# Performance work log

Hardware: AMD Instinct MI355X
Metric: run time of the kernel (lower is better)

## Reference

```python
import jax, jax.numpy as jnp
import numpy as np

B, N, DIM, H = 2, 4096, 1024, 16
LAT = 1024
CTX = N - LAT            # 3072 context tokens
SEG = 12                 # num_segments
CHUNK = CTX // SEG       # 256 tokens per segment
D = DIM // H             # 64 head dim
SCALE = D ** -0.5
LN_EPS = 1e-5
NEG = float(-np.finfo(np.float32).max)


def _split_heads(t):  # [B, N, DIM] -> [(B*H), N, D]
    return t.reshape(B, N, H, D).transpose(0, 2, 1, 3).reshape(B * H, N, D)


def _merge_heads(t):  # [(B*H), n, D] -> [B, n, DIM]
    n = t.shape[1]
    return t.reshape(B, H, n, D).transpose(0, 2, 1, 3).reshape(B, n, DIM)


def _layernorm(t, g, b):  # LN over last dim (head dim)
    mu = t.mean(-1, keepdims=True)
    var = ((t - mu) ** 2).mean(-1, keepdims=True)
    return (t - mu) * jax.lax.rsqrt(var + LN_EPS) * g + b


def _rope(t):  # rotary embedding over full head dim, half-split rotate
    pos = jnp.arange(N, dtype=jnp.float32)
    inv = 1.0 / (10000.0 ** (jnp.arange(0, D, 2, dtype=jnp.float32) / D))
    freqs = pos[:, None] * inv[None, :]          # [N, D/2]
    emb = jnp.concatenate([freqs, freqs], -1)    # [N, D]
    cos, sin = jnp.cos(emb), jnp.sin(emb)
    rot = jnp.concatenate([-t[..., D // 2:], t[..., : D // 2]], -1)
    return t * cos + rot * sin


def setup_inputs() -> dict:
    key = jax.random.key(0)
    ks = jax.random.split(key, 4)
    s = 0.02
    return {
        "x": jax.random.normal(ks[0], (B, N, DIM), jnp.float32),
        "Wq": jax.random.normal(ks[1], (DIM, DIM), jnp.float32) * s,
        "Wkv": jax.random.normal(ks[2], (DIM, DIM), jnp.float32) * s,
        "Wo": jax.random.normal(ks[3], (DIM, DIM), jnp.float32) * s,
        "bo": jnp.zeros((DIM,), jnp.float32),
        "ln_g": jnp.ones((D,), jnp.float32),
        "ln_b": jnp.zeros((D,), jnp.float32),
    }


def reference(x, Wq, Wkv, Wo, bo, ln_g, ln_b):
    q = _split_heads(x @ Wq)    # [(BH), N, D]
    kv = _split_heads(x @ Wkv)  # [(BH), N, D]
    q, kv = _rope(q), _rope(kv)

    lkv = _layernorm(kv, ln_g, ln_b)  # normalized keys/values, full seq

    q_lat = q[:, CTX:] * SCALE                                   # [(BH), LAT, D]
    q_ctx = (q[:, :CTX] * SCALE).reshape(B * H, SEG, CHUNK, D)   # segmented ctx queries
    lkv_ctx = lkv[:, :CTX].reshape(B * H, SEG, CHUNK, D)         # segmented norm'd kv

    # latent queries: full attention over all N positions, causal among latents
    lsim = jnp.einsum('bid,bjd->bij', q_lat, lkv)                # [(BH), LAT, N]
    tri = jnp.triu(jnp.ones((LAT, LAT), bool), 1)
    lat_block = jnp.where(tri, NEG, lsim[:, :, CTX:])
    lsim = jnp.concatenate([lsim[:, :, :CTX], lat_block], axis=-1)
    attn = jax.nn.softmax(lsim, axis=-1)
    out_lat = jnp.einsum('bij,bjd->bid', attn, lkv)              # [(BH), LAT, D]

    # context queries: block-diagonal segmented local attention (non-causal)
    sim_ctx = jnp.einsum('bsid,bsjd->bsij', q_ctx, lkv_ctx)      # [(BH), SEG, CHUNK, CHUNK]
    attn_ctx = jax.nn.softmax(sim_ctx, axis=-1)
    out_ctx = jnp.einsum('bsij,bsjd->bsid', attn_ctx, lkv_ctx).reshape(B * H, CTX, D)

    out = jnp.concatenate([_merge_heads(out_ctx), _merge_heads(out_lat)], axis=1)
    return out @ Wo + bo
```

## Files before the change

### kernel.cpp

```cpp
#include <hip/hip_runtime.h>
#include <math.h>

#define NB_B 2
#define NB_N 4096
#define NB_DIM 1024
#define NB_H 16
#define NB_D 64
#define NB_CTX 3072
#define NSPLIT 4
#define QSCALE 0.18033688011112042f
#define NEGF -3.0e38f

typedef __attribute__((ext_vector_type(8))) short short8;
typedef __attribute__((ext_vector_type(4))) short s4v;
typedef __attribute__((ext_vector_type(4))) float f32x4;

#if __has_builtin(__builtin_amdgcn_mfma_f32_16x16x16bf16_1k)
__device__ __forceinline__ f32x4 mfma16(s4v a, s4v b, f32x4 c) {
  return __builtin_amdgcn_mfma_f32_16x16x16bf16_1k(a, b, c, 0, 0, 0);
}
#else
__device__ __forceinline__ f32x4 mfma16(s4v a, s4v b, f32x4 c) {
  f32x4 d;
  asm volatile("v_mfma_f32_16x16x16_bf16 %0, %1, %2, %3"
               : "=v"(d) : "v"(a), "v"(b), "v"(c));
  return d;
}
#endif

__device__ __forceinline__ unsigned short f2bf(float f) {
  union { float f; unsigned u; } v; v.f = f;
  unsigned r = v.u + 0x7fffu + ((v.u >> 16) & 1u);
  return (unsigned short)(r >> 16);
}

__device__ __forceinline__ unsigned int cvtpk(float a, float b) {
  unsigned int r;
  asm("v_cvt_pk_bf16_f32 %0, %1, %2" : "=v"(r) : "v"(a), "v"(b));
  return r;
}

__device__ __forceinline__ void async16(const void* g, void* l) {
  typedef const unsigned int __attribute__((address_space(1)))* gas_t;
  typedef unsigned int __attribute__((address_space(3)))* las_t;
  __builtin_amdgcn_global_load_lds((gas_t)(unsigned long long)g,
                                   (las_t)(unsigned)(unsigned long long)l,
                                   16, 0, 0);
}

__global__ __launch_bounds__(256) void k_prep(
    const float* __restrict__ x,
    const float* __restrict__ Wq, const float* __restrict__ Wkv, const float* __restrict__ Wo,
    unsigned short* __restrict__ xb, unsigned short* __restrict__ WqkvT,
    unsigned short* __restrict__ WoT, float2* __restrict__ tab)
{
  __shared__ float tile[64][65];
  const int bx = blockIdx.x, tid = threadIdx.x;
  if (bx < 2048) {
    const float4* x4 = (const float4*)x;
    ushort4* xb4 = (ushort4*)xb;
    const int n4 = (NB_B * NB_N * NB_DIM) / 4;
    for (int i = bx * 256 + tid; i < n4; i += 2048 * 256) {
      float4 v = x4[i];
      ushort4 o;
      o.x = f2bf(v.x); o.y = f2bf(v.y); o.z = f2bf(v.z); o.w = f2bf(v.w);
      xb4[i] = o;
    }
  } else if (bx < 2816) {
    int idx = bx - 2048;
    int z = idx >> 8, rem = idx & 255;
    const float* W; unsigned short* out;
    if (z == 0)      { W = Wq;  out = WqkvT; }
    else if (z == 1) { W = Wkv; out = WqkvT + 1024 * 1024; }
    else             { W = Wo;  out = WoT; }
    int c0 = (rem & 15) * 64, k0 = (rem >> 4) * 64;
    int tx = tid & 63, ty = tid >> 6;
    #pragma unroll
    for (int i = 0; i < 16; ++i) {
      int k = ty + i * 4;
      tile[k][tx] = W[(long)(k0 + k) * 1024 + c0 + tx];
    }
    __syncthreads();
    #pragma unroll
    for (int i = 0; i < 16; ++i) {
      int c = ty + i * 4;
      out[(long)(c0 + c) * 1024 + k0 + tx] = f2bf(tile[tx][c]);
    }
  } else {
    int idx = (bx - 2816) * 256 + tid;
    int n = idx >> 5, fi = idx & 31;
    float inv = exp2f(-(float)fi * (13.287712379549449f / 32.0f));
    float ang = (float)n * inv;
    float s, c;
    sincosf(ang, &s, &c);
    tab[idx] = make_float2(c, s);
  }
}

__global__ __launch_bounds__(256) void k_gemm_qkv(
    const unsigned short* __restrict__ A,
    const unsigned short* __restrict__ Bt,
    unsigned short* __restrict__ qf,
    unsigned short* __restrict__ lkvp,
    const float2* __restrict__ tab,
    const float* __restrict__ ln_g,
    const float* __restrict__ ln_b)
{
  __shared__ unsigned short As[128 * 32];
  __shared__ unsigned short Bs[128 * 32];
  const int tid = threadIdx.x;
  const int w = tid >> 6, lane = tid & 63;
  const int wr = w >> 1, wc = w & 1;
  const int quad = lane >> 4, l15 = lane & 15;
  const long tm = (long)blockIdx.y * 128, tn = (long)blockIdx.x * 128;
  const int K = 1024;

  f32x4 acc[4][4];
  #pragma unroll
  for (int i = 0; i < 4; ++i)
    #pragma unroll
    for (int j = 0; j < 4; ++j)
      acc[i][j] = (f32x4){0.f, 0.f, 0.f, 0.f};

  const unsigned short* Ag0 = A + (tm + w * 16 + (lane >> 2)) * K + (lane & 3) * 8;
  const unsigned short* Bg0 = Bt + (tn + w * 16 + (lane >> 2)) * K + (lane & 3) * 8;
  const unsigned short* Ag1 = Ag0 + (long)64 * K;
  const unsigned short* Bg1 = Bg0 + (long)64 * K;
  unsigned short* Al0 = &As[(w * 16) * 32];
  unsigned short* Al1 = &As[(64 + w * 16) * 32];
  unsigned short* Bl0 = &Bs[(w * 16) * 32];
  unsigned short* Bl1 = &Bs[(64 + w * 16) * 32];

  for (int k0 = 0; k0 < K; k0 += 32) {
    __syncthreads();
    async16(Ag0 + k0, Al0);
    async16(Ag1 + k0, Al1);
    async16(Bg0 + k0, Bl0);
    async16(Bg1 + k0, Bl1);
    __syncthreads();
    short8 af[4], bfr[4];
    #pragma unroll
    for (int i = 0; i < 4; ++i)
      af[i] = *(const short8*)&As[(wr * 64 + i * 16 + l15) * 32 + quad * 8];
    #pragma unroll
    for (int j = 0; j < 4; ++j)
      bfr[j] = *(const short8*)&Bs[(wc * 64 + j * 16 + l15) * 32 + quad * 8];
    #pragma unroll
    for (int i = 0; i < 4; ++i)
      #pragma unroll
      for (int j = 0; j < 4; ++j)
        acc[i][j] = __builtin_amdgcn_mfma_f32_16x16x32_bf16(af[i], bfr[j], acc[i][j], 0, 0, 0);
  }

  const int col_base = (int)tn + wc * 64;
  const bool is_q = col_base < 1024;
  const int hh = (col_base & 1023) >> 6;
  unsigned short* dst = is_q ? qf : lkvp;
  float g_ln[4], b_ln[4];
  #pragma unroll
  for (int j = 0; j < 4; ++j) { g_ln[j] = ln_g[j * 16 + l15]; b_ln[j] = ln_b[j * 16 + l15]; }

  const int row_base = (int)tm + wr * 64;
  #pragma unroll
  for (int i = 0; i < 4; ++i) {
    #pragma unroll
    for (int r = 0; r < 4; ++r) {
      const int row = row_base + i * 16 + quad * 4 + r;
      const int n = row & 4095, b = row >> 12;
      const float2 cs0 = tab[n * 32 + l15];
      const float2 cs1 = tab[n * 32 + 16 + l15];
      float val[4];
      #pragma unroll
      for (int j = 0; j < 4; ++j) {
        float t = acc[i][j][r], pt = acc[i][j ^ 2][r];
        float2 cs = (j & 1) ? cs1 : cs0;
        float rot = (j < 2) ? -pt : pt;
        val[j] = t * cs.x + rot * cs.y;
      }
      unsigned short* orow = dst + ((long)(b * 16 + hh) * NB_N + n) * 64;
      if (is_q) {
        #pragma unroll
        for (int j = 0; j < 4; ++j)
          orow[j * 16 + l15] = f2bf(val[j] * QSCALE);
      } else {
        float s = val[0] + val[1] + val[2] + val[3];
        #pragma unroll
        for (int o = 1; o < 16; o <<= 1) s += __shfl_xor(s, o);
        const float mu = s * 0.015625f;
        float dv[4], vs = 0.f;
        #pragma unroll
        for (int j = 0; j < 4; ++j) { dv[j] = val[j] - mu; vs += dv[j] * dv[j]; }
        #pragma unroll
        for (int o = 1; o < 16; o <<= 1) vs += __shfl_xor(vs, o);
        const float rr = rsqrtf(vs * 0.015625f + 1e-5f);
        #pragma unroll
        for (int j = 0; j < 4; ++j)
          orow[j * 16 + l15] = f2bf(dv[j] * rr * g_ln[j] + b_ln[j]);
      }
    }
  }
}

__global__ __launch_bounds__(256) void k_gemm_bt(
    const unsigned short* __restrict__ A,
    const unsigned short* __restrict__ Bt,
    float* __restrict__ C,
    const float* __restrict__ bias,
    int K, int ldc)
{
  __shared__ unsigned short As[128 * 32];
  __shared__ unsigned short Bs[128 * 32];
  const int tid = threadIdx.x;
  const int w = tid >> 6, lane = tid & 63;
  const int wr = w >> 1, wc = w & 1;
  const int quad = lane >> 4, l15 = lane & 15;
  const long tm = (long)blockIdx.y * 128, tn = (long)blockIdx.x * 128;

  f32x4 acc[4][4];
  #pragma unroll
  for (int i = 0; i < 4; ++i)
    #pragma unroll
    for (int j = 0; j < 4; ++j)
      acc[i][j] = (f32x4){0.f, 0.f, 0.f, 0.f};

  const unsigned short* Ag0 = A + (tm + w * 16 + (lane >> 2)) * K + (lane & 3) * 8;
  const unsigned short* Bg0 = Bt + (tn + w * 16 + (lane >> 2)) * K + (lane & 3) * 8;
  const unsigned short* Ag1 = Ag0 + (long)64 * K;
  const unsigned short* Bg1 = Bg0 + (long)64 * K;
  unsigned short* Al0 = &As[(w * 16) * 32];
  unsigned short* Al1 = &As[(64 + w * 16) * 32];
  unsigned short* Bl0 = &Bs[(w * 16) * 32];
  unsigned short* Bl1 = &Bs[(64 + w * 16) * 32];

  for (int k0 = 0; k0 < K; k0 += 32) {
    __syncthreads();
    async16(Ag0 + k0, Al0);
    async16(Ag1 + k0, Al1);
    async16(Bg0 + k0, Bl0);
    async16(Bg1 + k0, Bl1);
    __syncthreads();
    short8 af[4], bfr[4];
    #pragma unroll
    for (int i = 0; i < 4; ++i)
      af[i] = *(const short8*)&As[(wr * 64 + i * 16 + l15) * 32 + quad * 8];
    #pragma unroll
    for (int j = 0; j < 4; ++j)
      bfr[j] = *(const short8*)&Bs[(wc * 64 + j * 16 + l15) * 32 + quad * 8];
    #pragma unroll
    for (int i = 0; i < 4; ++i)
      #pragma unroll
      for (int j = 0; j < 4; ++j)
        acc[i][j] = __builtin_amdgcn_mfma_f32_16x16x32_bf16(af[i], bfr[j], acc[i][j], 0, 0, 0);
  }

  #pragma unroll
  for (int j = 0; j < 4; ++j) {
    const long col = tn + wc * 64 + j * 16 + l15;
    const float bv = bias ? bias[col] : 0.0f;
    #pragma unroll
    for (int i = 0; i < 4; ++i) {
      #pragma unroll
      for (int r = 0; r < 4; ++r) {
        const long row = tm + wr * 64 + i * 16 + quad * 4 + r;
        C[row * ldc + col] = acc[i][j][r] + bv;
      }
    }
  }
}


__device__ __forceinline__ void stage_kv(
    unsigned short* __restrict__ Ksn, unsigned short* __restrict__ Vtn,
    const int kp, const int sdc, const uint4& gA, const uint4& gB)
{
  *(uint4*)&Ksn[(2 * kp) * 72 + sdc * 8] = gA;
  *(uint4*)&Ksn[(2 * kp + 1) * 72 + sdc * 8] = gB;
  const unsigned int* wA = (const unsigned int*)&gA;
  const unsigned int* wB = (const unsigned int*)&gB;
  #pragma unroll
  for (int jw = 0; jw < 4; ++jw) {
    const unsigned int lo = __builtin_amdgcn_perm(wB[jw], wA[jw], 0x05040100u);
    const unsigned int hi = __builtin_amdgcn_perm(wB[jw], wA[jw], 0x07060302u);
    const int d0 = sdc * 8 + jw * 2;
    const int xo = (2 * kp) ^ (d0 & 56);
    *(unsigned int*)&Vtn[d0 * 72 + xo] = lo;
    *(unsigned int*)&Vtn[(d0 + 1) * 72 + xo] = hi;
  }
}

#define NB_PACK(QG, SUB)                                               \
  _Pragma("unroll")                                                    \
  for (int k4 = 0; k4 < 4; ++k4) {                                     \
    const float p0 = __builtin_amdgcn_exp2f(st[QG][k4][0] SUB);        \
    const float p1 = __builtin_amdgcn_exp2f(st[QG][k4][1] SUB);        \
    const float p2 = __builtin_amdgcn_exp2f(st[QG][k4][2] SUB);        \
    const float p3 = __builtin_amdgcn_exp2f(st[QG][k4][3] SUB);        \
    pk[QG][k4][0] = cvtpk(p0, p1);                                     \
    pk[QG][k4][1] = cvtpk(p2, p3);                                     \
  }

__device__ __forceinline__ void attn_tile(
    const unsigned short* __restrict__ Ks, const unsigned short* __restrict__ Vt,
    unsigned short* __restrict__ Ksn, unsigned short* __restrict__ Vtn,
    const int kt, const int kt1, const int kstart, const bool latent, const int q0lat,
    const int w, const int quad, const int l15, const int kp, const int sdc,
    const unsigned short* __restrict__ kbase,
    uint4& gA, uint4& gB, const short8 (&qfr)[2][2],
    f32x4 (&ot)[2][4], f32x4 (&lacc)[2], float& miu, float& thr)
{
  const int key0 = kstart + kt * 64;
  __syncthreads();

  if (kt + 1 < kt1) {
    stage_kv(Ksn, Vtn, kp, sdc, gA, gB);
    if (kt + 2 < kt1) {
      const long k2 = (long)(key0 + 128);
      gA = *(const uint4*)(kbase + (k2 + 2 * kp) * 64 + sdc * 8);
      gB = *(const uint4*)(kbase + (k2 + 2 * kp + 1) * 64 + sdc * 8);
    }
  }

  f32x4 st[2][4];
  #pragma unroll
  for (int qg = 0; qg < 2; ++qg)
    #pragma unroll
    for (int k4 = 0; k4 < 4; ++k4)
      st[qg][k4] = (f32x4){0.f, 0.f, 0.f, 0.f};
  #pragma unroll
  for (int kc = 0; kc < 2; ++kc) {
    short8 kf[4];
    #pragma unroll
    for (int k4 = 0; k4 < 4; ++k4)
      kf[k4] = *(const short8*)&Ks[(k4 * 16 + l15) * 72 + kc * 32 + quad * 8];
    #pragma unroll
    for (int qg = 0; qg < 2; ++qg)
      #pragma unroll
      for (int k4 = 0; k4 < 4; ++k4)
        st[qg][k4] = __builtin_amdgcn_mfma_f32_16x16x32_bf16(kf[k4], qfr[qg][kc], st[qg][k4], 0, 0, 0);
  }

  if (latent && key0 + 63 >= NB_CTX) {
    #pragma unroll
    for (int qg = 0; qg < 2; ++qg) {
      const int qrow = q0lat + w * 32 + qg * 16 + l15;
      #pragma unroll
      for (int k4 = 0; k4 < 4; ++k4)
        #pragma unroll
        for (int r = 0; r < 4; ++r) {
          const int kl = key0 + k4 * 16 + quad * 4 + r - NB_CTX;
          if (kl > qrow) st[qg][k4][r] = NEGF;
        }
    }
  }

  float mx = st[0][0][0];
  #pragma unroll
  for (int qg = 0; qg < 2; ++qg)
    #pragma unroll
    for (int k4 = 0; k4 < 4; ++k4)
      mx = fmaxf(mx, fmaxf(fmaxf(st[qg][k4][0], st[qg][k4][1]),
                           fmaxf(st[qg][k4][2], st[qg][k4][3])));

  unsigned int pk[2][4][2];
  if (miu == 0.f) {
    NB_PACK(0, )
    NB_PACK(1, )
  } else {
    NB_PACK(0, - miu)
    NB_PACK(1, - miu)
  }

  const s4v vones = { (short)0x3F80, (short)0x3F80, (short)0x3F80, (short)0x3F80 };
  #pragma unroll
  for (int k4 = 0; k4 < 4; ++k4) {
    s4v vf[4];
    const int kb = k4 * 16 + quad * 4;
    #pragma unroll
    for (int dt = 0; dt < 4; ++dt) {
      const int row = dt * 16 + l15;
      vf[dt] = *(const s4v*)&Vt[row * 72 + (kb ^ (row & 56))];
    }
    #pragma unroll
    for (int qg = 0; qg < 2; ++qg) {
      s4v pf;
      ((unsigned int*)&pf)[0] = pk[qg][k4][0];
      ((unsigned int*)&pf)[1] = pk[qg][k4][1];
      lacc[qg] = mfma16(vones, pf, lacc[qg]);
      #pragma unroll
      for (int dt = 0; dt < 4; ++dt)
        ot[qg][dt] = mfma16(vf[dt], pf, ot[qg][dt]);
    }
  }

  if (__builtin_expect(__any(mx > thr), 0)) {
    #pragma unroll
    for (int o = 1; o < 64; o <<= 1) mx = fmaxf(mx, __shfl_xor(mx, o));
    const float c = __builtin_amdgcn_exp2f(miu - mx);
    miu = mx; thr = mx + 8.f;
    #pragma unroll
    for (int qg = 0; qg < 2; ++qg) {
      lacc[qg][0] *= c; lacc[qg][1] *= c; lacc[qg][2] *= c; lacc[qg][3] *= c;
      #pragma unroll
      for (int dt = 0; dt < 4; ++dt) {
        ot[qg][dt][0] *= c; ot[qg][dt][1] *= c;
        ot[qg][dt][2] *= c; ot[qg][dt][3] *= c;
      }
    }
  }
}

__global__ __launch_bounds__(256) void k_attn(
    const unsigned short* __restrict__ qf,
    const unsigned short* __restrict__ lkv,
    unsigned short* __restrict__ attn_out,
    float* __restrict__ Opart,
    float* __restrict__ mpart,
    float* __restrict__ lpart)
{
  __shared__ unsigned short smem[18432];
  unsigned short* const Ks0 = smem;
  unsigned short* const Vt0 = smem + 4608;
  unsigned short* const Ks1 = smem + 9216;
  unsigned short* const Vt1 = smem + 13824;

  const int tid = threadIdx.x;
  const int w = tid >> 6, lane = tid & 63;
  const int quad = lane >> 4, l15 = lane & 15;

  const int bx = blockIdx.x;
  int bh, q0tok, kstart, kt0, kt1, q0lat, s6 = 0, qb = 0;
  bool latent;
  if (bx < 256 * NSPLIT) {
    latent = true;
    qb = bx / NSPLIT;
    s6 = bx % NSPLIT;
    bh = qb >> 3;
    q0lat = (qb & 7) * 128;
    q0tok = NB_CTX + q0lat;
    kstart = 0;
    const int nkt = (NB_CTX + q0lat + 128) >> 6;
    const int hk = nkt >> 1;
    kt0 = 2 * ((s6 * hk) / NSPLIT);
    kt1 = 2 * (((s6 + 1) * hk) / NSPLIT);
  } else {
    latent = false;
    int idx = bx - 256 * NSPLIT;
    bh = idx / 24;
    int r2 = idx % 24;
    int seg = r2 >> 1;
    q0lat = 0;
    q0tok = seg * 256 + (r2 & 1) * 128;
    kstart = seg * 256;
    kt0 = 0; kt1 = 4;
  }

  const unsigned short* qbase = qf + ((long)bh * NB_N + q0tok) * 64;
  const unsigned short* kbase = lkv + (long)bh * NB_N * 64;

  short8 qfr[2][2];
  #pragma unroll
  for (int qg = 0; qg < 2; ++qg)
    #pragma unroll
    for (int kc = 0; kc < 2; ++kc)
      qfr[qg][kc] = *(const short8*)(qbase + (w * 32 + qg * 16 + l15) * 64 + kc * 32 + quad * 8);

  const int kp = tid >> 3, sdc = tid & 7;

  uint4 gA, gB;
  {
    const int key0 = kstart + kt0 * 64;
    gA = *(const uint4*)(kbase + (long)(key0 + 2 * kp) * 64 + sdc * 8);
    gB = *(const uint4*)(kbase + (long)(key0 + 2 * kp + 1) * 64 + sdc * 8);
  }
  stage_kv(Ks0, Vt0, kp, sdc, gA, gB);
  {
    const int key1 = kstart + (kt0 + 1) * 64;
    gA = *(const uint4*)(kbase + (long)(key1 + 2 * kp) * 64 + sdc * 8);
    gB = *(const uint4*)(kbase + (long)(key1 + 2 * kp + 1) * 64 + sdc * 8);
  }

  f32x4 ot[2][4];
  f32x4 lacc[2];
  float miu = 0.f, thr = 8.f;
  #pragma unroll
  for (int qg = 0; qg < 2; ++qg) {
    #pragma unroll
    for (int dt = 0; dt < 4; ++dt) ot[qg][dt] = (f32x4){0.f, 0.f, 0.f, 0.f};
    lacc[qg] = (f32x4){0.f, 0.f, 0.f, 0.f};
  }

  for (int kt = kt0; kt < kt1; kt += 2) {
    attn_tile(Ks0, Vt0, Ks1, Vt1, kt,     kt1, kstart, latent, q0lat,
              w, quad, l15, kp, sdc, kbase, gA, gB, qfr, ot, lacc, miu, thr);
    attn_tile(Ks1, Vt1, Ks0, Vt0, kt + 1, kt1, kstart, latent, q0lat,
              w, quad, l15, kp, sdc, kbase, gA, gB, qfr, ot, lacc, miu, thr);
  }

  __syncthreads();
  if (latent) {
    const long pb = (long)(s6 * 256 + qb);
    if (quad == 0) {
      #pragma unroll
      for (int qg = 0; qg < 2; ++qg) {
        mpart[pb * 128 + w * 32 + qg * 16 + l15] = miu;
        lpart[pb * 128 + w * 32 + qg * 16 + l15] = lacc[qg][0];
      }
    }
    float* obase = Opart + pb * 8192;
    #pragma unroll
    for (int qg = 0; qg < 2; ++qg) {
      const int q = w * 32 + qg * 16 + l15;
      #pragma unroll
      for (int dt = 0; dt < 4; ++dt)
        #pragma unroll
        for (int r = 0; r < 4; ++r)
          obase[(dt * 16 + quad * 4 + r) * 128 + q] = ot[qg][dt][r];
    }
  } else {
    #pragma unroll
    for (int qg = 0; qg < 2; ++qg) {
      const float inv = 1.0f / lacc[qg][0];
      const int q = w * 32 + qg * 16 + l15;
      #pragma unroll
      for (int dt = 0; dt < 4; ++dt)
        #pragma unroll
        for (int r = 0; r < 4; ++r)
          smem[q * 72 + dt * 16 + quad * 4 + r] = f2bf(ot[qg][dt][r] * inv);
    }
    __syncthreads();
    const int qrow = tid >> 1, half = tid & 1;
    const int b_ = bh >> 4, h_ = bh & 15;
    unsigned short* orow = attn_out + ((long)b_ * NB_N + q0tok + qrow) * NB_DIM + h_ * 64 + half * 32;
    #pragma unroll
    for (int v = 0; v < 4; ++v)
      *(uint4*)(orow + v * 8) = *(const uint4*)&smem[qrow * 72 + half * 32 + v * 8];
  }
}

__global__ __launch_bounds__(256) void k_combine(
    const float* __restrict__ Opart, const float* __restrict__ mpart,
    const float* __restrict__ lpart, unsigned short* __restrict__ attn_out)
{
  __shared__ unsigned short lds[9216];
  const int qb = blockIdx.x;
  const int bh = qb >> 3, qt = qb & 7;
  const int b = bh >> 4, h = bh & 15;
  const int t = threadIdx.x;
  const int qq = t & 31;
  const int dg = t >> 5;

  float m[NSPLIT][4], l[NSPLIT][4];
  float mstar[4];
  #pragma unroll
  for (int qi = 0; qi < 4; ++qi) mstar[qi] = NEGF;
  #pragma unroll
  for (int s = 0; s < NSPLIT; ++s) {
    #pragma unroll
    for (int qi = 0; qi < 4; ++qi) {
      m[s][qi] = mpart[(s * 256 + qb) * 128 + qq * 4 + qi];
      l[s][qi] = lpart[(s * 256 + qb) * 128 + qq * 4 + qi];
      mstar[qi] = fmaxf(mstar[qi], m[s][qi]);
    }
  }
  float inv[4];
  #pragma unroll
  for (int qi = 0; qi < 4; ++qi) {
    float lsum = 0.f;
    #pragma unroll
    for (int s = 0; s < NSPLIT; ++s)
      lsum += __builtin_amdgcn_exp2f(m[s][qi] - mstar[qi]) * l[s][qi];
    inv[qi] = 1.0f / lsum;
  }

  float o[8][4];
  #pragma unroll
  for (int dd = 0; dd < 8; ++dd)
    #pragma unroll
    for (int qi = 0; qi < 4; ++qi) o[dd][qi] = 0.f;
  #pragma unroll
  for (int s = 0; s < NSPLIT; ++s) {
    float wgt[4];
    #pragma unroll
    for (int qi = 0; qi < 4; ++qi)
      wgt[qi] = __builtin_amdgcn_exp2f(m[s][qi] - mstar[qi]);
    const float* base = Opart + (long)(s * 256 + qb) * 8192;
    #pragma unroll
    for (int dd = 0; dd < 8; ++dd) {
      float4 v = *(const float4*)(base + (dg * 8 + dd) * 128 + qq * 4);
      o[dd][0] += wgt[0] * v.x; o[dd][1] += wgt[1] * v.y;
      o[dd][2] += wgt[2] * v.z; o[dd][3] += wgt[3] * v.w;
    }
  }
  #pragma unroll
  for (int qi = 0; qi < 4; ++qi) {
    ushort4 u0, u1;
    u0.x = f2bf(o[0][qi] * inv[qi]); u0.y = f2bf(o[1][qi] * inv[qi]);
    u0.z = f2bf(o[2][qi] * inv[qi]); u0.w = f2bf(o[3][qi] * inv[qi]);
    u1.x = f2bf(o[4][qi] * inv[qi]); u1.y = f2bf(o[5][qi] * inv[qi]);
    u1.z = f2bf(o[6][qi] * inv[qi]); u1.w = f2bf(o[7][qi] * inv[qi]);
    *(ushort4*)&lds[(qq * 4 + qi) * 72 + dg * 8] = u0;
    *(ushort4*)&lds[(qq * 4 + qi) * 72 + dg * 8 + 4] = u1;
  }
  __syncthreads();
  const int qrow = t >> 1, half = t & 1;
  unsigned short* orow = attn_out + ((long)b * NB_N + NB_CTX + qt * 128 + qrow) * NB_DIM + h * 64 + half * 32;
  #pragma unroll
  for (int v = 0; v < 4; ++v)
    *(uint4*)(orow + v * 8) = *(const uint4*)&lds[qrow * 72 + half * 32 + v * 8];
}

extern "C" void kernel_launch(void* const* d_in, const int* in_sizes, int n_in,
                              void* d_out, int out_size, void* d_ws, size_t ws_size,
                              hipStream_t stream)
{
  const float* x    = (const float*)d_in[0];
  const float* Wq   = (const float*)d_in[1];
  const float* Wkv  = (const float*)d_in[2];
  const float* Wo   = (const float*)d_in[3];
  const float* bo   = (const float*)d_in[4];
  const float* ln_g = (const float*)d_in[5];
  const float* ln_b = (const float*)d_in[6];
  float* out = (float*)d_out;

  char* ws = (char*)d_ws;
  unsigned short* xb    = (unsigned short*)(ws);
  unsigned short* WqkvT = (unsigned short*)(ws + (size_t)(16 << 20));
  unsigned short* WoT   = (unsigned short*)(ws + (size_t)(20 << 20));
  float2*         tab   = (float2*)        (ws + (size_t)(22 << 20));
  unsigned short* qfb   = (unsigned short*)(ws + (size_t)(24 << 20));
  unsigned short* lkv   = (unsigned short*)(ws + (size_t)(40 << 20));
  unsigned short* aout  = (unsigned short*)(ws + (size_t)(56 << 20));
  float*          Opart = (float*)         (ws + (size_t)(72 << 20));
  float*          mpart = (float*)         (ws + (size_t)(112 << 20));
  float*          lpart = (float*)         (ws + (size_t)(113 << 20));

  hipLaunchKernelGGL(k_prep, dim3(3328), dim3(256), 0, stream,
                     x, Wq, Wkv, Wo, xb, WqkvT, WoT, tab);
  hipLaunchKernelGGL(k_gemm_qkv, dim3(16, 64), dim3(256), 0, stream,
                     xb, WqkvT, qfb, lkv, tab, ln_g, ln_b);
  hipLaunchKernelGGL(k_attn, dim3(256 * NSPLIT + 768), dim3(256), 0, stream,
                     qfb, lkv, aout, Opart, mpart, lpart);
  hipLaunchKernelGGL(k_combine, dim3(256), dim3(256), 0, stream,
                     Opart, mpart, lpart, aout);
  hipLaunchKernelGGL(k_gemm_bt, dim3(8, 64), dim3(256), 0, stream,
                     aout, WoT, out, bo, 1024, 1024);
}
```

Measured before the change: 266.1 us.

## Store split-K attention partials as normalized fp16 and delay next-tile staging

Latent split partial outputs are now normalized by their own row sum and written as fp16, row-major per query, instead of unnormalized fp32 in transposed layout. This halves partial-buffer traffic, and the combine kernel is simplified to read contiguous rows without an LDS transpose, weighting each split by exp(m - m*) times l. Separately, staging of the next K/V tile into LDS is moved after the current tile's MFMA work, so the global-load latency can overlap compute. Storing partials in fp16 adds some rounding error.

```diff
diff --git a/kernel.cpp b/kernel.cpp
--- a/kernel.cpp
+++ b/kernel.cpp
@@ -14,6 +14,7 @@
 typedef __attribute__((ext_vector_type(8))) short short8;
 typedef __attribute__((ext_vector_type(4))) short s4v;
 typedef __attribute__((ext_vector_type(4))) float f32x4;
+typedef __fp16 fp16x2 __attribute__((ext_vector_type(2)));
 
 #if __has_builtin(__builtin_amdgcn_mfma_f32_16x16x16bf16_1k)
 __device__ __forceinline__ f32x4 mfma16(s4v a, s4v b, f32x4 c) {
@@ -38,6 +39,12 @@
   unsigned int r;
   asm("v_cvt_pk_bf16_f32 %0, %1, %2" : "=v"(r) : "v"(a), "v"(b));
   return r;
+}
+
+__device__ __forceinline__ unsigned int pkh(float a, float b) {
+  union { fp16x2 h; unsigned int u; } cv;
+  cv.h = __builtin_amdgcn_cvt_pkrtz(a, b);
+  return cv.u;
 }
 
 __device__ __forceinline__ void async16(const void* g, void* l) {
@@ -311,15 +318,6 @@
   const int key0 = kstart + kt * 64;
   __syncthreads();
 
-  if (kt + 1 < kt1) {
-    stage_kv(Ksn, Vtn, kp, sdc, gA, gB);
-    if (kt + 2 < kt1) {
-      const long k2 = (long)(key0 + 128);
-      gA = *(const uint4*)(kbase + (k2 + 2 * kp) * 64 + sdc * 8);
-      gB = *(const uint4*)(kbase + (k2 + 2 * kp + 1) * 64 + sdc * 8);
-    }
-  }
-
   f32x4 st[2][4];
   #pragma unroll
   for (int qg = 0; qg < 2; ++qg)
@@ -392,6 +390,15 @@
     }
   }
 
+  if (kt + 1 < kt1) {
+    stage_kv(Ksn, Vtn, kp, sdc, gA, gB);
+    if (kt + 2 < kt1) {
+      const long k2 = (long)(key0 + 128);
+      gA = *(const uint4*)(kbase + (k2 + 2 * kp) * 64 + sdc * 8);
+      gB = *(const uint4*)(kbase + (k2 + 2 * kp + 1) * 64 + sdc * 8);
+    }
+  }
+
   if (__builtin_expect(__any(mx > thr), 0)) {
     #pragma unroll
     for (int o = 1; o < 64; o <<= 1) mx = fmaxf(mx, __shfl_xor(mx, o));
@@ -413,7 +420,7 @@
     const unsigned short* __restrict__ qf,
     const unsigned short* __restrict__ lkv,
     unsigned short* __restrict__ attn_out,
-    float* __restrict__ Opart,
+    unsigned short* __restrict__ Opart,
     float* __restrict__ mpart,
     float* __restrict__ lpart)
 {
@@ -506,15 +513,18 @@
         lpart[pb * 128 + w * 32 + qg * 16 + l15] = lacc[qg][0];
       }
     }
-    float* obase = Opart + pb * 8192;
+    unsigned short* obase = Opart + pb * 8192;
     #pragma unroll
     for (int qg = 0; qg < 2; ++qg) {
+      const float inv = 1.0f / lacc[qg][0];
       const int q = w * 32 + qg * 16 + l15;
       #pragma unroll
-      for (int dt = 0; dt < 4; ++dt)
-        #pragma unroll
-        for (int r = 0; r < 4; ++r)
-          obase[(dt * 16 + quad * 4 + r) * 128 + q] = ot[qg][dt][r];
+      for (int dt = 0; dt < 4; ++dt) {
+        uint2 u;
+        u.x = pkh(ot[qg][dt][0] * inv, ot[qg][dt][1] * inv);
+        u.y = pkh(ot[qg][dt][2] * inv, ot[qg][dt][3] * inv);
+        *(uint2*)&obase[q * 64 + dt * 16 + quad * 4] = u;
+      }
     }
   } else {
     #pragma unroll
@@ -538,75 +548,62 @@
 }
 
 __global__ __launch_bounds__(256) void k_combine(
-    const float* __restrict__ Opart, const float* __restrict__ mpart,
+    const unsigned short* __restrict__ Opart, const float* __restrict__ mpart,
     const float* __restrict__ lpart, unsigned short* __restrict__ attn_out)
 {
-  __shared__ unsigned short lds[9216];
   const int qb = blockIdx.x;
   const int bh = qb >> 3, qt = qb & 7;
   const int b = bh >> 4, h = bh & 15;
   const int t = threadIdx.x;
-  const int qq = t & 31;
-  const int dg = t >> 5;
-
-  float m[NSPLIT][4], l[NSPLIT][4];
-  float mstar[4];
-  #pragma unroll
-  for (int qi = 0; qi < 4; ++qi) mstar[qi] = NEGF;
+  const int q = t >> 1;
+  const int dh = (t & 1) * 32;
+
+  float m[NSPLIT], l[NSPLIT], mstar = NEGF;
   #pragma unroll
   for (int s = 0; s < NSPLIT; ++s) {
-    #pragma unroll
-    for (int qi = 0; qi < 4; ++qi) {
-      m[s][qi] = mpart[(s * 256 + qb) * 128 + qq * 4 + qi];
-      l[s][qi] = lpart[(s * 256 + qb) * 128 + qq * 4 + qi];
-      mstar[qi] = fmaxf(mstar[qi], m[s][qi]);
-    }
-  }
-  float inv[4];
-  #pragma unroll
-  for (int qi = 0; qi < 4; ++qi) {
-    float lsum = 0.f;
-    #pragma unroll
-    for (int s = 0; s < NSPLIT; ++s)
-      lsum += __builtin_amdgcn_exp2f(m[s][qi] - mstar[qi]) * l[s][qi];
-    inv[qi] = 1.0f / lsum;
-  }
-
-  float o[8][4];
-  #pragma unroll
-  for (int dd = 0; dd < 8; ++dd)
-    #pragma unroll
-    for (int qi = 0; qi < 4; ++qi) o[dd][qi] = 0.f;
+    m[s] = mpart[(s * 256 + qb) * 128 + q];
+    l[s] = lpart[(s * 256 + qb) * 128 + q];
+    mstar = fmaxf(mstar, m[s]);
+  }
+  float wsum = 0.f, ws[NSPLIT];
   #pragma unroll
   for (int s = 0; s < NSPLIT; ++s) {
-    float wgt[4];
-    #pragma unroll
-    for (int qi = 0; qi < 4; ++qi)
-      wgt[qi] = __builtin_amdgcn_exp2f(m[s][qi] - mstar[qi]);
-    const float* base = Opart + (long)(s * 256 + qb) * 8192;
-    #pragma unroll
-    for (int dd = 0; dd < 8; ++dd) {
-      float4 v = *(const float4*)(base + (dg * 8 + dd) * 128 + qq * 4);
-      o[dd][0] += wgt[0] * v.x; o[dd][1] += wgt[1] * v.y;
-      o[dd][2] += wgt[2] * v.z; o[dd][3] += wgt[3] * v.w;
-    }
-  }
-  #pragma unroll
-  for (int qi = 0; qi < 4; ++qi) {
-    ushort4 u0, u1;
-    u0.x = f2bf(o[0][qi] * inv[qi]); u0.y = f2bf(o[1][qi] * inv[qi]);
-    u0.z = f2bf(o[2][qi] * inv[qi]); u0.w = f2bf(o[3][qi] * inv[qi]);
-    u1.x = f2bf(o[4][qi] * inv[qi]); u1.y = f2bf(o[5][qi] * inv[qi]);
-    u1.z = f2bf(o[6][qi] * inv[qi]); u1.w = f2bf(o[7][qi] * inv[qi]);
-    *(ushort4*)&lds[(qq * 4 + qi) * 72 + dg * 8] = u0;
-    *(ushort4*)&lds[(qq * 4 + qi) * 72 + dg * 8 + 4] = u1;
-  }
-  __syncthreads();
-  const int qrow = t >> 1, half = t & 1;
-  unsigned short* orow = attn_out + ((long)b * NB_N + NB_CTX + qt * 128 + qrow) * NB_DIM + h * 64 + half * 32;
-  #pragma unroll
-  for (int v = 0; v < 4; ++v)
-    *(uint4*)(orow + v * 8) = *(const uint4*)&lds[qrow * 72 + half * 32 + v * 8];
+    ws[s] = __builtin_amdgcn_exp2f(m[s] - mstar) * l[s];
+    wsum += ws[s];
+  }
+  const float inv = 1.0f / wsum;
+
+  float acc[32];
+  #pragma unroll
+  for (int d = 0; d < 32; ++d) acc[d] = 0.f;
+
+  #pragma unroll
+  for (int s = 0; s < NSPLIT; ++s) {
+    const unsigned short* base = Opart + ((long)(s * 256 + qb)) * 8192 + q * 64 + dh;
+    const float wv = ws[s];
+    #pragma unroll
+    for (int v = 0; v < 4; ++v) {
+      uint4 u = *(const uint4*)(base + v * 8);
+      const unsigned int uw[4] = {u.x, u.y, u.z, u.w};
+      #pragma unroll
+      for (int e = 0; e < 4; ++e) {
+        union { unsigned int u; fp16x2 h; } cv; cv.u = uw[e];
+        acc[v * 8 + e * 2]     += wv * (float)cv.h[0];
+        acc[v * 8 + e * 2 + 1] += wv * (float)cv.h[1];
+      }
+    }
+  }
+
+  unsigned short* orow = attn_out + ((long)b * NB_N + NB_CTX + qt * 128 + q) * NB_DIM + h * 64 + dh;
+  #pragma unroll
+  for (int v = 0; v < 4; ++v) {
+    uint4 u;
+    u.x = (unsigned)f2bf(acc[v * 8 + 0] * inv) | ((unsigned)f2bf(acc[v * 8 + 1] * inv) << 16);
+    u.y = (unsigned)f2bf(acc[v * 8 + 2] * inv) | ((unsigned)f2bf(acc[v * 8 + 3] * inv) << 16);
+    u.z = (unsigned)f2bf(acc[v * 8 + 4] * inv) | ((unsigned)f2bf(acc[v * 8 + 5] * inv) << 16);
+    u.w = (unsigned)f2bf(acc[v * 8 + 6] * inv) | ((unsigned)f2bf(acc[v * 8 + 7] * inv) << 16);
+    *(uint4*)(orow + v * 8) = u;
+  }
 }
 
 extern "C" void kernel_launch(void* const* d_in, const int* in_sizes, int n_in,
@@ -630,7 +627,7 @@
   unsigned short* qfb   = (unsigned short*)(ws + (size_t)(24 << 20));
   unsigned short* lkv   = (unsigned short*)(ws + (size_t)(40 << 20));
   unsigned short* aout  = (unsigned short*)(ws + (size_t)(56 << 20));
-  float*          Opart = (float*)         (ws + (size_t)(72 << 20));
+  unsigned short* Opart = (unsigned short*)(ws + (size_t)(72 << 20));
   float*          mpart = (float*)         (ws + (size_t)(112 << 20));
   float*          lpart = (float*)         (ws + (size_t)(113 << 20));
 
```

After: 263.8 us. Within noise of the previous version (-0.9%).
